# Kernel tuning notes

Hardware: AMD Instinct MI355X
Metric: run time of the kernel (lower is better)

Reference implementation:

```python
import jax, jax.numpy as jnp
import numpy as np

B, S, HID, H, D = 4, 1024, 2048, 16, 128
ROT = D // 2  # GLM 2D rotary: rotary dim is half the head dim (64)


def _rope_tables(seq_len, dim, base=10000.0):
    # dim = ROT; inv_freq over dim//2 frequencies, emb = cat(freqs, freqs)
    inv_freq = 1.0 / (base ** (jnp.arange(0, dim, 2, dtype=jnp.float32) / dim))
    t = jnp.arange(seq_len, dtype=jnp.float32)
    freqs = jnp.einsum('s,f->sf', t, inv_freq)          # [S, dim//2]
    emb = jnp.concatenate([freqs, freqs], axis=-1)       # [S, dim]
    return jnp.cos(emb), jnp.sin(emb)


def _rotate_half(x):
    x1, x2 = jnp.split(x, 2, axis=-1)
    return jnp.concatenate([-x2, x1], axis=-1)


def _apply_rope(x, cos, sin, pos_id):
    # x: [B,H,S,ROT]; pos_id: [B,S]; tables: [S,ROT]
    c = cos[pos_id][:, None, :, :]  # [B,1,S,ROT]
    s = sin[pos_id][:, None, :, :]
    return x * c + _rotate_half(x) * s


def setup_inputs() -> dict:
    key = jax.random.key(0)
    ks = jax.random.split(key, 12)
    w = 0.02
    inp = {
        'query': jax.random.normal(ks[0], (B, S, HID), jnp.float32),
        'key': jax.random.normal(ks[1], (B, S, HID), jnp.float32),
        'value': jax.random.normal(ks[2], (B, S, HID), jnp.float32),
        'mask': jnp.zeros((B, 1, S, S), jnp.float32),
        'position_bias': jax.random.normal(ks[3], (1, H, S, S), jnp.float32) * 0.1,
        'prev_attn': jax.random.normal(ks[4], (B, H, S, S), jnp.float32) * 0.1,
        'position_ids': jax.random.randint(ks[5], (B, 2, S), 0, S, jnp.int32),
        'Wq': jax.random.normal(ks[6], (HID, HID), jnp.float32) * w,
        'bq': jnp.zeros((HID,), jnp.float32),
        'Wk': jax.random.normal(ks[7], (HID, HID), jnp.float32) * w,
        'bk': jnp.zeros((HID,), jnp.float32),
        'Wv': jax.random.normal(ks[8], (HID, HID), jnp.float32) * w,
        'bv': jnp.zeros((HID,), jnp.float32),
        'Wo': jax.random.normal(ks[9], (HID, HID), jnp.float32) * w,
        'bo': jnp.zeros((HID,), jnp.float32),
    }
    return inp


def reference(query, key, value, mask, position_bias, prev_attn,
              Wq, bq, Wk, bk, Wv, bv, Wo, bo, position_ids):
    # QKV projections -> [B,H,S,D]
    def proj(x, W, b):
        return (x @ W.T + b).reshape(B, S, H, D).transpose(0, 2, 1, 3)
    q = proj(query, Wq, bq)
    k = proj(key, Wk, bk)
    v = proj(value, Wv, bv)

    # GLM 2D rotary: split head dim in halves, rope each with its own ids
    q1, q2 = jnp.split(q, 2, axis=-1)
    k1, k2 = jnp.split(k, 2, axis=-1)
    cos, sin = _rope_tables(S, ROT)
    pid = position_ids[:, 0, :]        # [B,S]
    bid = position_ids[:, 1, :]        # [B,S]
    q1 = _apply_rope(q1, cos, sin, pid)
    k1 = _apply_rope(k1, cos, sin, pid)
    q2 = _apply_rope(q2, cos, sin, bid)
    k2 = _apply_rope(k2, cos, sin, bid)
    q = jnp.concatenate([q1, q2], axis=-1)
    k = jnp.concatenate([k1, k2], axis=-1)

    scores = jnp.einsum('bhsd,bhtd->bhst', q, k)
    scores = scores + position_bias
    scores = scores / jnp.sqrt(jnp.float32(D))
    scores = scores + mask
    scores = scores + prev_attn          # residual attention accumulation
    prev_attn_out = scores
    probs = jax.nn.softmax(scores, axis=-1)
    ctx = jnp.einsum('bhst,bhtd->bhsd', probs, v)
    ctx = ctx.transpose(0, 2, 1, 3).reshape(B, S, HID)
    out = ctx @ Wo.T + bo
    return out, prev_attn_out
```

## Files before the change

### kernel.cpp

```cpp
#include <hip/hip_runtime.h>


#define B_  4
#define S_  1024
#define HID_ 2048
#define H_  16
#define D_  128
#define RSQRT_D 0.08838834764831845f

typedef _Float16 f16x8 __attribute__((ext_vector_type(8)));
typedef _Float16 f16x4 __attribute__((ext_vector_type(4)));
typedef float f32x4 __attribute__((ext_vector_type(4)));

#define MFMA16(a, b, c) __builtin_amdgcn_mfma_f32_16x16x32_f16(a, b, c, 0, 0, 0)

__device__ __forceinline__ void gll16(const void* g, void* l) {
  __builtin_amdgcn_global_load_lds(
      (const __attribute__((address_space(1))) void*)g,
      (__attribute__((address_space(3))) void*)l, 16, 0, 0);
}

__global__ __launch_bounds__(256) void cvt_all_kernel(
    const float* __restrict__ w0, const float* __restrict__ w1,
    const float* __restrict__ w2, const float* __restrict__ w3,
    const float* __restrict__ x0, const float* __restrict__ x1,
    const float* __restrict__ x2,
    _Float16* __restrict__ dw0, _Float16* __restrict__ dw1,
    _Float16* __restrict__ dw2, _Float16* __restrict__ dw3,
    _Float16* __restrict__ dx0, _Float16* __restrict__ dx1,
    _Float16* __restrict__ dx2,
    float* __restrict__ tcos, float* __restrict__ tsin) {
  if (blockIdx.x >= 20480) {
    const int i = (blockIdx.x - 20480) * 256 + threadIdx.x;
    const int pos = i >> 5, j = i & 31;
    const float inv = expf(-(float)j * (9.210340371976184f / 32.0f));
    const float ang = (float)pos * inv;
    tcos[i] = cosf(ang);
    tsin[i] = sinf(ang);
    return;
  }
  const int i = blockIdx.x * blockDim.x + threadIdx.x;
  const float* src;
  _Float16* dst;
  int off;
  if (i < 2097152) {
    const int seg = i >> 19;
    off = i & 524287;
    src = (seg == 0) ? w0 : (seg == 1) ? w1 : (seg == 2) ? w2 : w3;
    dst = (seg == 0) ? dw0 : (seg == 1) ? dw1 : (seg == 2) ? dw2 : dw3;
  } else {
    const int j = i - 2097152;
    const int seg = j >> 20;
    off = j & 1048575;
    src = (seg == 0) ? x0 : (seg == 1) ? x1 : x2;
    dst = (seg == 0) ? dx0 : (seg == 1) ? dx1 : dx2;
  }
  const f32x4* in4 = (const f32x4*)src;
  f32x4 a = in4[(size_t)off * 2], b = in4[(size_t)off * 2 + 1];
  f16x8 v;
  v[0] = (_Float16)a[0]; v[1] = (_Float16)a[1]; v[2] = (_Float16)a[2]; v[3] = (_Float16)a[3];
  v[4] = (_Float16)b[0]; v[5] = (_Float16)b[1]; v[6] = (_Float16)b[2]; v[7] = (_Float16)b[3];
  *(f16x8*)(dst + (size_t)off * 8) = v;
}

__device__ __forceinline__ void stage_tile_256(
    const _Float16* __restrict__ A, const _Float16* __restrict__ Bw,
    int m0, int n0, int k0s, _Float16* ad, _Float16* bd, int tid) {
#pragma unroll
  for (int i = 0; i < 4; ++i) {
    const int e = i * 4096 + tid * 8;
    const int rrow = e >> 6;
    const int rcol = (e & 63) ^ ((rrow & 7) << 3);
    gll16(A + (size_t)(m0 + rrow) * HID_ + k0s + rcol, ad + e);
    gll16(Bw + (size_t)(n0 + rrow) * HID_ + k0s + rcol, bd + e);
  }
}

__global__ __launch_bounds__(512) void proj_qkv_kernel(
    const _Float16* __restrict__ Xq, const _Float16* __restrict__ Xk,
    const _Float16* __restrict__ Xv,
    const _Float16* __restrict__ Wq, const _Float16* __restrict__ Wk,
    const _Float16* __restrict__ Wv,
    const float* __restrict__ bq, const float* __restrict__ bk,
    const float* __restrict__ bv,
    _Float16* __restrict__ oq, _Float16* __restrict__ ok,
    _Float16* __restrict__ ovt,
    const int* __restrict__ pids, const float* __restrict__ tcos,
    const float* __restrict__ tsin) {
  constexpr int K = HID_;
  constexpr int BK = 64;
  constexpr int NK = K / BK;
  __shared__ _Float16 As[2][256 * BK];
  __shared__ _Float16 Bs[2][256 * BK];

  const int tid = threadIdx.x;
  const int gbid = (blockIdx.x & 7) * 48 + (blockIdx.x >> 3);
  const int seg = gbid / 128;
  const int bid = gbid % 128;
  const _Float16* A  = (seg == 0) ? Xq : (seg == 1) ? Xk : Xv;
  const _Float16* Bw = (seg == 0) ? Wq : (seg == 1) ? Wk : Wv;
  const float*  bias = (seg == 0) ? bq : (seg == 1) ? bk : bv;

  const int tm = bid >> 3, tn = bid & 7;
  const int m0 = tm * 256, n0 = tn * 256;
  const int w = tid >> 6, l = tid & 63;
  const int wr = w >> 2, wc = w & 3;
  const int lr = l & 15, lh = l >> 4;
  const int swz = (lr & 7) << 3;

  f32x4 acc[8][4] = {};

  stage_tile_256(A, Bw, m0, n0, 0, &As[0][0], &Bs[0][0], tid);

  for (int j = 0; j < NK; ++j) {
    const _Float16* as = &As[j & 1][0];
    const _Float16* bs = &Bs[j & 1][0];

    if (j + 1 < NK) {
      stage_tile_256(A, Bw, m0, n0, (j + 1) * BK,
                     &As[(j + 1) & 1][0], &Bs[(j + 1) & 1][0], tid);
      asm volatile("s_waitcnt vmcnt(8)" ::: "memory");
    } else {
      asm volatile("s_waitcnt vmcnt(0)" ::: "memory");
    }
    __builtin_amdgcn_sched_barrier(0);
    __builtin_amdgcn_s_barrier();

#pragma unroll
    for (int p = 0; p < 4; ++p) {
      const int qm = p & 1, kk = p >> 1;
      if (p > 0) __builtin_amdgcn_s_barrier();
      f16x8 af[4], bf[4];
#pragma unroll
      for (int i = 0; i < 4; ++i)
        af[i] = *(const f16x8*)(as + (wr * 128 + (qm * 4 + i) * 16 + lr) * BK +
                                ((kk * 32 + lh * 8) ^ swz));
#pragma unroll
      for (int ni = 0; ni < 4; ++ni)
        bf[ni] = *(const f16x8*)(bs + (wc * 64 + ni * 16 + lr) * BK +
                                 ((kk * 32 + lh * 8) ^ swz));
      asm volatile("s_waitcnt lgkmcnt(0)" ::: "memory");
      __builtin_amdgcn_sched_barrier(0);
      __builtin_amdgcn_s_setprio(1);
#pragma unroll
      for (int i = 0; i < 4; ++i)
#pragma unroll
        for (int ni = 0; ni < 4; ++ni)
          acc[qm * 4 + i][ni] = MFMA16(af[i], bf[ni], acc[qm * 4 + i][ni]);
      __builtin_amdgcn_s_setprio(0);
    }
    __builtin_amdgcn_s_barrier();
  }

  if (seg == 2) {
#pragma unroll
    for (int mi = 0; mi < 8; ++mi)
#pragma unroll
      for (int ni = 0; ni < 4; ++ni) {
        const int col = n0 + wc * 64 + ni * 16 + lr;
        const float bb = bias[col];
        const int h = col >> 7, hd = col & 127;
#pragma unroll
        for (int r = 0; r < 4; ++r) {
          const int row = m0 + wr * 128 + mi * 16 + lh * 4 + r;
          const int b = row >> 10, s = row & 1023;
          ovt[(((size_t)(b * H_ + h)) * D_ + hd) * S_ + s] =
              (_Float16)(acc[mi][ni][r] + bb);
        }
      }
  } else {
    _Float16* out = (seg == 0) ? oq : ok;
    const int sel = wc & 1;
#pragma unroll
    for (int mi = 0; mi < 8; ++mi) {
#pragma unroll
      for (int r = 0; r < 4; ++r) {
        const int row = m0 + wr * 128 + mi * 16 + lh * 4 + r;
        const int b = row >> 10, s = row & 1023;
        const int pos = pids[b * 2 * S_ + sel * S_ + s];
#pragma unroll
        for (int ni = 0; ni < 2; ++ni) {
          const int col = n0 + wc * 64 + ni * 16 + lr;
          const int jf = ni * 16 + lr;
          const float c = tcos[pos * 32 + jf];
          const float sn = tsin[pos * 32 + jf];
          const float x1 = acc[mi][ni][r] + bias[col];
          const float x2 = acc[mi][ni + 2][r] + bias[col + 32];
          const int h = col >> 7, hd = col & 127;
          const size_t base = (((size_t)(b * H_ + h)) * S_ + s) * D_;
          out[base + hd] = (_Float16)(x1 * c - x2 * sn);
          out[base + hd + 32] = (_Float16)(x2 * c + x1 * sn);
        }
      }
    }
  }
}

__global__ __launch_bounds__(256) void proj_out_kernel(
    const _Float16* __restrict__ A, const _Float16* __restrict__ Bw,
    const float* __restrict__ bias, float* __restrict__ out) {
  constexpr int N = HID_, K = HID_;
  constexpr int BK = 64;
  __shared__ _Float16 As[128 * BK];
  __shared__ _Float16 Bs[128 * BK];

  const int tid = threadIdx.x;
  const int bid = (blockIdx.x & 7) * 64 + (blockIdx.x >> 3);
  const int tm = bid >> 4, tn = bid & 15;
  const int m0 = tm * 128, n0 = tn * 128;
  const int w = tid >> 6, l = tid & 63;
  const int mw = (w >> 1) * 64, nw = (w & 1) * 64;
  const int lr = l & 15, lh = l >> 4;

  f32x4 acc[4][4] = {};

  for (int kt = 0; kt < K / BK; ++kt) {
    const int k0 = kt * BK;
    __syncthreads();
#pragma unroll
    for (int i = 0; i < 4; ++i) {
      const int e = i * 2048 + tid * 8;
      gll16(A + (size_t)(m0 + (e >> 6)) * K + k0 + (e & 63), As + e);
      gll16(Bw + (size_t)(n0 + (e >> 6)) * K + k0 + (e & 63), Bs + e);
    }
    asm volatile("s_waitcnt vmcnt(0)" ::: "memory");
    __syncthreads();
#pragma unroll
    for (int kk = 0; kk < 2; ++kk) {
      f16x8 af[4], bf[4];
#pragma unroll
      for (int mi = 0; mi < 4; ++mi)
        af[mi] = *(const f16x8*)(As + (mw + mi * 16 + lr) * BK + kk * 32 + lh * 8);
#pragma unroll
      for (int ni = 0; ni < 4; ++ni)
        bf[ni] = *(const f16x8*)(Bs + (nw + ni * 16 + lr) * BK + kk * 32 + lh * 8);
#pragma unroll
      for (int mi = 0; mi < 4; ++mi)
#pragma unroll
        for (int ni = 0; ni < 4; ++ni)
          acc[mi][ni] = MFMA16(af[mi], bf[ni], acc[mi][ni]);
    }
  }

#pragma unroll
  for (int mi = 0; mi < 4; ++mi)
#pragma unroll
    for (int ni = 0; ni < 4; ++ni) {
      const int col = n0 + nw + ni * 16 + lr;
      const float bb = bias[col];
#pragma unroll
      for (int r = 0; r < 4; ++r) {
        const int row = m0 + mw + mi * 16 + lh * 4 + r;
        out[(size_t)row * N + col] = acc[mi][ni][r] + bb;
      }
    }
}

__global__ __launch_bounds__(256) void flash_kernel(
    const _Float16* __restrict__ q, const _Float16* __restrict__ k,
    const _Float16* __restrict__ vt, const float* __restrict__ pbias,
    const float* __restrict__ maskp, const float* __restrict__ prev,
    float* __restrict__ scores, _Float16* __restrict__ ctx) {
  constexpr int BT = 64;
  __shared__ _Float16 KsBuf[2][BT * D_];
  __shared__ _Float16 VTsBuf[2][D_ * BT];
  __shared__ _Float16 Ps[4][16 * BT];

  const int tid = threadIdx.x, w = tid >> 6, l = tid & 63;
  const int lr = l & 15, lh = l >> 4;
  const int sid = (blockIdx.x & 7) * 128 + (blockIdx.x >> 3);
  const int qt = sid & 15, byh = sid >> 4;
  const int b = byh >> 4, h = byh & 15;
  const size_t plane = (size_t)byh;
  const int q0 = qt * 64 + w * 16;
  const int qrow = q0 + lr;
  const int swz = (lr & 7) << 3;

  const float* prow  = prev  + (plane * S_ + qrow) * S_;
  const float* pbrow = pbias + ((size_t)h * S_ + qrow) * S_;
  const float* mrow  = maskp + ((size_t)b * S_ + qrow) * S_;
  float*       srow  = scores + (plane * S_ + qrow) * S_;
  const _Float16* kpl = k  + plane * S_ * D_;
  const _Float16* vpl = vt + plane * D_ * S_;

  f16x8 qa[4];
#pragma unroll
  for (int kk = 0; kk < 4; ++kk)
    qa[kk] = *(const f16x8*)(q + (plane * S_ + qrow) * D_ + kk * 32 + lh * 8);

  f32x4 o[8] = {};
  float m_r = -1e30f, l_r = 0.0f;

  _Float16* ksA = &KsBuf[0][0];
  _Float16* ksB = &KsBuf[1][0];
  _Float16* vtA = &VTsBuf[0][0];
  _Float16* vtB = &VTsBuf[1][0];

#pragma unroll
  for (int i = 0; i < 4; ++i) {
    const int e = i * 2048 + tid * 8;
    const int krow = e >> 7;
    gll16(kpl + (size_t)krow * D_ + ((e & 127) ^ ((krow & 7) << 3)), ksA + e);
    const int vrow = e >> 6;
    gll16(vpl + (size_t)vrow * S_ + ((e & 63) ^ ((vrow & 7) << 3)), vtA + e);
  }
  __syncthreads();

  for (int tt = 0; tt < S_ / BT; ++tt) {
    const int t0 = tt * BT;

    f32x4 pv4[4], pb4[4], mk4[4];
#pragma unroll
    for (int nt = 0; nt < 4; ++nt) {
      const int toff = t0 + nt * 16 + lh * 4;
      pv4[nt] = __builtin_nontemporal_load((const f32x4*)(prow + toff));
      pb4[nt] = *(const f32x4*)(pbrow + toff);
      mk4[nt] = *(const f32x4*)(mrow + toff);
    }
    if (tt < S_ / BT - 1) {
      const int t1 = t0 + BT;
#pragma unroll
      for (int i = 0; i < 4; ++i) {
        const int e = i * 2048 + tid * 8;
        const int krow = e >> 7;
        gll16(kpl + (size_t)(t1 + krow) * D_ + ((e & 127) ^ ((krow & 7) << 3)), ksB + e);
        const int vrow = e >> 6;
        gll16(vpl + (size_t)vrow * S_ + t1 + ((e & 63) ^ ((vrow & 7) << 3)), vtB + e);
      }
    }

    f32x4 sa[4] = {};
    __builtin_amdgcn_s_setprio(1);
#pragma unroll
    for (int nt = 0; nt < 4; ++nt)
#pragma unroll
      for (int kk = 0; kk < 4; ++kk) {
        const int row = nt * 16 + lr;
        f16x8 kb = *(const f16x8*)(ksA + row * D_ + ((kk * 32 + lh * 8) ^ swz));
        sa[nt] = MFMA16(kb, qa[kk], sa[nt]);
      }
    __builtin_amdgcn_s_setprio(0);

#pragma unroll
    for (int nt = 0; nt < 4; ++nt) {
      const int toff = t0 + nt * 16 + lh * 4;
      f32x4 sc4 = (sa[nt] + pb4[nt]) * RSQRT_D + mk4[nt] + pv4[nt];
      __builtin_nontemporal_store(sc4, (f32x4*)(srow + toff));
      sa[nt] = sc4;
    }

    float tmx = -1e30f;
#pragma unroll
    for (int nt = 0; nt < 4; ++nt)
#pragma unroll
      for (int r = 0; r < 4; ++r) tmx = fmaxf(tmx, sa[nt][r]);
    tmx = fmaxf(tmx, __shfl_xor(tmx, 16));
    tmx = fmaxf(tmx, __shfl_xor(tmx, 32));
    if (!__all(tmx <= m_r + 8.0f)) {
      const float newm = fmaxf(m_r, tmx);
      const float al = __expf(m_r - newm);
      m_r = newm;
      l_r *= al;
#pragma unroll
      for (int nd = 0; nd < 8; ++nd) o[nd] *= al;
    }
    float ts = 0.0f;
#pragma unroll
    for (int nt = 0; nt < 4; ++nt)
#pragma unroll
      for (int r = 0; r < 4; ++r) {
        const float pe = __expf(sa[nt][r] - m_r);
        sa[nt][r] = pe;
        ts += pe;
      }
    ts += __shfl_xor(ts, 16);
    ts += __shfl_xor(ts, 32);
    l_r += ts;

    _Float16* pw = &Ps[w][0];
#pragma unroll
    for (int nt = 0; nt < 4; ++nt) {
      f16x4 pk;
      pk[0] = (_Float16)sa[nt][0]; pk[1] = (_Float16)sa[nt][1];
      pk[2] = (_Float16)sa[nt][2]; pk[3] = (_Float16)sa[nt][3];
      *(f16x4*)(pw + lr * BT + ((nt * 16 + lh * 4) ^ swz)) = pk;
    }

    __builtin_amdgcn_s_setprio(1);
#pragma unroll
    for (int kk2 = 0; kk2 < 2; ++kk2) {
      const f16x8 pa = *(const f16x8*)(pw + lr * BT + ((kk2 * 32 + lh * 8) ^ swz));
#pragma unroll
      for (int nd = 0; nd < 8; ++nd) {
        const int vr = nd * 16 + lr;
        const f16x8 vb = *(const f16x8*)(vtA + vr * BT + ((kk2 * 32 + lh * 8) ^ swz));
        o[nd] = MFMA16(vb, pa, o[nd]);
      }
    }
    __builtin_amdgcn_s_setprio(0);

    asm volatile("s_waitcnt vmcnt(4)" ::: "memory");
    __builtin_amdgcn_s_barrier();
    _Float16* t1p = ksA; ksA = ksB; ksB = t1p;
    _Float16* t2p = vtA; vtA = vtB; vtB = t2p;
  }

  const float inv_l = 1.0f / l_r;
  _Float16* crow = ctx + ((size_t)(b * S_) + qrow) * HID_ + h * D_;
#pragma unroll
  for (int nd = 0; nd < 8; ++nd) {
    f16x4 cv;
#pragma unroll
    for (int r = 0; r < 4; ++r) cv[r] = (_Float16)(o[nd][r] * inv_l);
    *(f16x4*)(crow + nd * 16 + lh * 4) = cv;
  }
}

extern "C" void kernel_launch(void* const* d_in, const int* in_sizes, int n_in,
                              void* d_out, int out_size, void* d_ws, size_t ws_size,
                              hipStream_t stream) {
  const float* query = (const float*)d_in[0];
  const float* key_i = (const float*)d_in[1];
  const float* value = (const float*)d_in[2];
  const float* maskp = (const float*)d_in[3];
  const float* pbias = (const float*)d_in[4];
  const float* prev  = (const float*)d_in[5];
  const int*   pids  = (const int*)d_in[6];
  const float* Wq = (const float*)d_in[7];
  const float* bq = (const float*)d_in[8];
  const float* Wk = (const float*)d_in[9];
  const float* bk = (const float*)d_in[10];
  const float* Wv = (const float*)d_in[11];
  const float* bv = (const float*)d_in[12];
  const float* Wo = (const float*)d_in[13];
  const float* bo = (const float*)d_in[14];

  char* ws = (char*)d_ws;
  const size_t OFF_TCOS = 0;
  const size_t OFF_TSIN = 131072;
  const size_t OFF_W    = 262144;
  const size_t OFF_X    = OFF_W + 4ull * 8388608;
  const size_t OFF_Q    = OFF_X + 3ull * 16777216;
  const size_t OFF_K    = OFF_Q + 16777216;
  const size_t OFF_VT   = OFF_K + 16777216;
  const size_t OFF_CTX  = OFF_X + 16777216;

  float* tcos = (float*)(ws + OFF_TCOS);
  float* tsin = (float*)(ws + OFF_TSIN);
  _Float16* Wq16 = (_Float16*)(ws + OFF_W);
  _Float16* Wk16 = (_Float16*)(ws + OFF_W + 8388608);
  _Float16* Wv16 = (_Float16*)(ws + OFF_W + 2ull * 8388608);
  _Float16* Wo16 = (_Float16*)(ws + OFF_W + 3ull * 8388608);
  _Float16* Xq16 = (_Float16*)(ws + OFF_X);
  _Float16* Xk16 = (_Float16*)(ws + OFF_X + 16777216);
  _Float16* Xv16 = (_Float16*)(ws + OFF_X + 2ull * 16777216);
  _Float16* q16  = (_Float16*)(ws + OFF_Q);
  _Float16* k16  = (_Float16*)(ws + OFF_K);
  _Float16* vt16 = (_Float16*)(ws + OFF_VT);
  _Float16* ctx16 = (_Float16*)(ws + OFF_CTX);

  float* out_f32 = (float*)d_out;
  float* scores  = (float*)d_out + 8388608;

  cvt_all_kernel<<<20608, 256, 0, stream>>>(Wq, Wk, Wv, Wo, query, key_i, value,
                                            Wq16, Wk16, Wv16, Wo16,
                                            Xq16, Xk16, Xv16, tcos, tsin);

  proj_qkv_kernel<<<384, 512, 0, stream>>>(Xq16, Xk16, Xv16,
                                           Wq16, Wk16, Wv16,
                                           bq, bk, bv,
                                           q16, k16, vt16,
                                           pids, tcos, tsin);

  flash_kernel<<<1024, 256, 0, stream>>>(q16, k16, vt16, pbias, maskp, prev,
                                         scores, ctx16);

  proj_out_kernel<<<512, 256, 0, stream>>>(ctx16, Wo16, bo, out_f32);
}
```

Baseline: 444.1 us.

## Shrink QKV GEMM tile to 256x128 and pipeline output projection

The QKV projection tile changes from 256x256 to 256x128, so the grid doubles to 768 blocks for better CU fill, and each warp now holds a 64x64 accumulator tile. The output projection is rewritten to use the same double-buffered, swizzled, async-LDS-load pipeline with 512 threads and 256x128 tiles, replacing the synchronous single-buffer loop. The goal is more occupancy and overlap of global loads with MFMA work. The cost is lower arithmetic intensity per tile in the QKV GEMM and fewer blocks (256) in the output GEMM.

```diff
diff --git a/kernel.cpp b/kernel.cpp
--- a/kernel.cpp
+++ b/kernel.cpp
@@ -60,10 +60,10 @@
   f16x8 v;
   v[0] = (_Float16)a[0]; v[1] = (_Float16)a[1]; v[2] = (_Float16)a[2]; v[3] = (_Float16)a[3];
   v[4] = (_Float16)b[0]; v[5] = (_Float16)b[1]; v[6] = (_Float16)b[2]; v[7] = (_Float16)b[3];
-  *(f16x8*)(dst + (size_t)off * 8) = v;
-}
-
-__device__ __forceinline__ void stage_tile_256(
+  *(f16x8*)(dst + (size_t)i * 0 + (size_t)off * 8) = v;
+}
+
+__device__ __forceinline__ void stage_tile_256x128(
     const _Float16* __restrict__ A, const _Float16* __restrict__ Bw,
     int m0, int n0, int k0s, _Float16* ad, _Float16* bd, int tid) {
 #pragma unroll
@@ -72,6 +72,12 @@
     const int rrow = e >> 6;
     const int rcol = (e & 63) ^ ((rrow & 7) << 3);
     gll16(A + (size_t)(m0 + rrow) * HID_ + k0s + rcol, ad + e);
+  }
+#pragma unroll
+  for (int i = 0; i < 2; ++i) {
+    const int e = i * 4096 + tid * 8;
+    const int rrow = e >> 6;
+    const int rcol = (e & 63) ^ ((rrow & 7) << 3);
     gll16(Bw + (size_t)(n0 + rrow) * HID_ + k0s + rcol, bd + e);
   }
 }
@@ -87,39 +93,39 @@
     _Float16* __restrict__ ovt,
     const int* __restrict__ pids, const float* __restrict__ tcos,
     const float* __restrict__ tsin) {
-  constexpr int K = HID_;
   constexpr int BK = 64;
-  constexpr int NK = K / BK;
+  constexpr int NK = HID_ / BK;
   __shared__ _Float16 As[2][256 * BK];
-  __shared__ _Float16 Bs[2][256 * BK];
+  __shared__ _Float16 Bs[2][128 * BK];
 
   const int tid = threadIdx.x;
-  const int gbid = (blockIdx.x & 7) * 48 + (blockIdx.x >> 3);
-  const int seg = gbid / 128;
-  const int bid = gbid % 128;
+  const int gbid = (blockIdx.x & 7) * 96 + (blockIdx.x >> 3);
+  const int seg = gbid >> 8;
+  const int bid = gbid & 255;
   const _Float16* A  = (seg == 0) ? Xq : (seg == 1) ? Xk : Xv;
   const _Float16* Bw = (seg == 0) ? Wq : (seg == 1) ? Wk : Wv;
   const float*  bias = (seg == 0) ? bq : (seg == 1) ? bk : bv;
 
-  const int tm = bid >> 3, tn = bid & 7;
-  const int m0 = tm * 256, n0 = tn * 256;
+  const int tm = bid >> 4, tn = bid & 15;
+  const int m0 = tm * 256, n0 = tn * 128;
   const int w = tid >> 6, l = tid & 63;
-  const int wr = w >> 2, wc = w & 3;
+  const int wr = w >> 1, wc = w & 1;
+  const int mw = wr * 64, nw = wc * 64;
   const int lr = l & 15, lh = l >> 4;
   const int swz = (lr & 7) << 3;
 
-  f32x4 acc[8][4] = {};
-
-  stage_tile_256(A, Bw, m0, n0, 0, &As[0][0], &Bs[0][0], tid);
+  f32x4 acc[4][4] = {};
+
+  stage_tile_256x128(A, Bw, m0, n0, 0, &As[0][0], &Bs[0][0], tid);
 
   for (int j = 0; j < NK; ++j) {
     const _Float16* as = &As[j & 1][0];
     const _Float16* bs = &Bs[j & 1][0];
 
     if (j + 1 < NK) {
-      stage_tile_256(A, Bw, m0, n0, (j + 1) * BK,
-                     &As[(j + 1) & 1][0], &Bs[(j + 1) & 1][0], tid);
-      asm volatile("s_waitcnt vmcnt(8)" ::: "memory");
+      stage_tile_256x128(A, Bw, m0, n0, (j + 1) * BK,
+                         &As[(j + 1) & 1][0], &Bs[(j + 1) & 1][0], tid);
+      asm volatile("s_waitcnt vmcnt(6)" ::: "memory");
     } else {
       asm volatile("s_waitcnt vmcnt(0)" ::: "memory");
     }
@@ -130,23 +136,23 @@
     for (int p = 0; p < 4; ++p) {
       const int qm = p & 1, kk = p >> 1;
       if (p > 0) __builtin_amdgcn_s_barrier();
-      f16x8 af[4], bf[4];
-#pragma unroll
-      for (int i = 0; i < 4; ++i)
-        af[i] = *(const f16x8*)(as + (wr * 128 + (qm * 4 + i) * 16 + lr) * BK +
+      f16x8 af[2], bf[4];
+#pragma unroll
+      for (int i = 0; i < 2; ++i)
+        af[i] = *(const f16x8*)(as + (mw + (qm * 2 + i) * 16 + lr) * BK +
                                 ((kk * 32 + lh * 8) ^ swz));
 #pragma unroll
       for (int ni = 0; ni < 4; ++ni)
-        bf[ni] = *(const f16x8*)(bs + (wc * 64 + ni * 16 + lr) * BK +
+        bf[ni] = *(const f16x8*)(bs + (nw + ni * 16 + lr) * BK +
                                  ((kk * 32 + lh * 8) ^ swz));
       asm volatile("s_waitcnt lgkmcnt(0)" ::: "memory");
       __builtin_amdgcn_sched_barrier(0);
       __builtin_amdgcn_s_setprio(1);
 #pragma unroll
-      for (int i = 0; i < 4; ++i)
+      for (int i = 0; i < 2; ++i)
 #pragma unroll
         for (int ni = 0; ni < 4; ++ni)
-          acc[qm * 4 + i][ni] = MFMA16(af[i], bf[ni], acc[qm * 4 + i][ni]);
+          acc[qm * 2 + i][ni] = MFMA16(af[i], bf[ni], acc[qm * 2 + i][ni]);
       __builtin_amdgcn_s_setprio(0);
     }
     __builtin_amdgcn_s_barrier();
@@ -154,15 +160,15 @@
 
   if (seg == 2) {
 #pragma unroll
-    for (int mi = 0; mi < 8; ++mi)
+    for (int mi = 0; mi < 4; ++mi)
 #pragma unroll
       for (int ni = 0; ni < 4; ++ni) {
-        const int col = n0 + wc * 64 + ni * 16 + lr;
+        const int col = n0 + nw + ni * 16 + lr;
         const float bb = bias[col];
         const int h = col >> 7, hd = col & 127;
 #pragma unroll
         for (int r = 0; r < 4; ++r) {
-          const int row = m0 + wr * 128 + mi * 16 + lh * 4 + r;
+          const int row = m0 + mw + mi * 16 + lh * 4 + r;
           const int b = row >> 10, s = row & 1023;
           ovt[(((size_t)(b * H_ + h)) * D_ + hd) * S_ + s] =
               (_Float16)(acc[mi][ni][r] + bb);
@@ -170,17 +176,17 @@
       }
   } else {
     _Float16* out = (seg == 0) ? oq : ok;
-    const int sel = wc & 1;
-#pragma unroll
-    for (int mi = 0; mi < 8; ++mi) {
+    const int sel = wc;
+#pragma unroll
+    for (int mi = 0; mi < 4; ++mi) {
 #pragma unroll
       for (int r = 0; r < 4; ++r) {
-        const int row = m0 + wr * 128 + mi * 16 + lh * 4 + r;
+        const int row = m0 + mw + mi * 16 + lh * 4 + r;
         const int b = row >> 10, s = row & 1023;
         const int pos = pids[b * 2 * S_ + sel * S_ + s];
 #pragma unroll
         for (int ni = 0; ni < 2; ++ni) {
-          const int col = n0 + wc * 64 + ni * 16 + lr;
+          const int col = n0 + nw + ni * 16 + lr;
           const int jf = ni * 16 + lr;
           const float c = tcos[pos * 32 + jf];
           const float sn = tsin[pos * 32 + jf];
@@ -196,50 +202,66 @@
   }
 }
 
-__global__ __launch_bounds__(256) void proj_out_kernel(
+__global__ __launch_bounds__(512) void proj_out_kernel(
     const _Float16* __restrict__ A, const _Float16* __restrict__ Bw,
     const float* __restrict__ bias, float* __restrict__ out) {
-  constexpr int N = HID_, K = HID_;
   constexpr int BK = 64;
-  __shared__ _Float16 As[128 * BK];
-  __shared__ _Float16 Bs[128 * BK];
+  constexpr int NK = HID_ / BK;
+  __shared__ _Float16 As[2][256 * BK];
+  __shared__ _Float16 Bs[2][128 * BK];
 
   const int tid = threadIdx.x;
-  const int bid = (blockIdx.x & 7) * 64 + (blockIdx.x >> 3);
-  const int tm = bid >> 4, tn = bid & 15;
-  const int m0 = tm * 128, n0 = tn * 128;
+  const int gbid = (blockIdx.x & 7) * 32 + (blockIdx.x >> 3);
+  const int tm = gbid >> 4, tn = gbid & 15;
+  const int m0 = tm * 256, n0 = tn * 128;
   const int w = tid >> 6, l = tid & 63;
-  const int mw = (w >> 1) * 64, nw = (w & 1) * 64;
+  const int wr = w >> 1, wc = w & 1;
+  const int mw = wr * 64, nw = wc * 64;
   const int lr = l & 15, lh = l >> 4;
+  const int swz = (lr & 7) << 3;
 
   f32x4 acc[4][4] = {};
 
-  for (int kt = 0; kt < K / BK; ++kt) {
-    const int k0 = kt * BK;
-    __syncthreads();
-#pragma unroll
-    for (int i = 0; i < 4; ++i) {
-      const int e = i * 2048 + tid * 8;
-      gll16(A + (size_t)(m0 + (e >> 6)) * K + k0 + (e & 63), As + e);
-      gll16(Bw + (size_t)(n0 + (e >> 6)) * K + k0 + (e & 63), Bs + e);
-    }
-    asm volatile("s_waitcnt vmcnt(0)" ::: "memory");
-    __syncthreads();
-#pragma unroll
-    for (int kk = 0; kk < 2; ++kk) {
-      f16x8 af[4], bf[4];
-#pragma unroll
-      for (int mi = 0; mi < 4; ++mi)
-        af[mi] = *(const f16x8*)(As + (mw + mi * 16 + lr) * BK + kk * 32 + lh * 8);
+  stage_tile_256x128(A, Bw, m0, n0, 0, &As[0][0], &Bs[0][0], tid);
+
+  for (int j = 0; j < NK; ++j) {
+    const _Float16* as = &As[j & 1][0];
+    const _Float16* bs = &Bs[j & 1][0];
+
+    if (j + 1 < NK) {
+      stage_tile_256x128(A, Bw, m0, n0, (j + 1) * BK,
+                         &As[(j + 1) & 1][0], &Bs[(j + 1) & 1][0], tid);
+      asm volatile("s_waitcnt vmcnt(6)" ::: "memory");
+    } else {
+      asm volatile("s_waitcnt vmcnt(0)" ::: "memory");
+    }
+    __builtin_amdgcn_sched_barrier(0);
+    __builtin_amdgcn_s_barrier();
+
+#pragma unroll
+    for (int p = 0; p < 4; ++p) {
+      const int qm = p & 1, kk = p >> 1;
+      if (p > 0) __builtin_amdgcn_s_barrier();
+      f16x8 af[2], bf[4];
+#pragma unroll
+      for (int i = 0; i < 2; ++i)
+        af[i] = *(const f16x8*)(as + (mw + (qm * 2 + i) * 16 + lr) * BK +
+                                ((kk * 32 + lh * 8) ^ swz));
 #pragma unroll
       for (int ni = 0; ni < 4; ++ni)
-        bf[ni] = *(const f16x8*)(Bs + (nw + ni * 16 + lr) * BK + kk * 32 + lh * 8);
-#pragma unroll
-      for (int mi = 0; mi < 4; ++mi)
+        bf[ni] = *(const f16x8*)(bs + (nw + ni * 16 + lr) * BK +
+                                 ((kk * 32 + lh * 8) ^ swz));
+      asm volatile("s_waitcnt lgkmcnt(0)" ::: "memory");
+      __builtin_amdgcn_sched_barrier(0);
+      __builtin_amdgcn_s_setprio(1);
+#pragma unroll
+      for (int i = 0; i < 2; ++i)
 #pragma unroll
         for (int ni = 0; ni < 4; ++ni)
-          acc[mi][ni] = MFMA16(af[mi], bf[ni], acc[mi][ni]);
-    }
+          acc[qm * 2 + i][ni] = MFMA16(af[i], bf[ni], acc[qm * 2 + i][ni]);
+      __builtin_amdgcn_s_setprio(0);
+    }
+    __builtin_amdgcn_s_barrier();
   }
 
 #pragma unroll
@@ -251,7 +273,7 @@
 #pragma unroll
       for (int r = 0; r < 4; ++r) {
         const int row = m0 + mw + mi * 16 + lh * 4 + r;
-        out[(size_t)row * N + col] = acc[mi][ni][r] + bb;
+        out[(size_t)row * HID_ + col] = acc[mi][ni][r] + bb;
       }
     }
 }
@@ -466,7 +488,7 @@
                                             Wq16, Wk16, Wv16, Wo16,
                                             Xq16, Xk16, Xv16, tcos, tsin);
 
-  proj_qkv_kernel<<<384, 512, 0, stream>>>(Xq16, Xk16, Xv16,
+  proj_qkv_kernel<<<768, 512, 0, stream>>>(Xq16, Xk16, Xv16,
                                            Wq16, Wk16, Wv16,
                                            bq, bk, bv,
                                            q16, k16, vt16,
@@ -475,5 +497,5 @@
   flash_kernel<<<1024, 256, 0, stream>>>(q16, k16, vt16, pbias, maskp, prev,
                                          scores, ctx16);
 
-  proj_out_kernel<<<512, 256, 0, stream>>>(ctx16, Wo16, bo, out_f32);
-}
+  proj_out_kernel<<<256, 512, 0, stream>>>(ctx16, Wo16, bo, out_f32);
+}
```

Result: no change. 452.2 us (+1.8%).
